# Kernel tuning notes

Hardware: AMD Instinct MI355X
Metric: run time of the kernel (lower is better)

The kernel has to match this reference:

```python
import jax, jax.numpy as jnp
import numpy as np
from math import factorial
from fractions import Fraction

MUL = 16          # multiplicity per irrep
LMAX = 2          # irreps l = 0, 1, 2
N_BATCH = 1024
RS = [(MUL, l, 0) for l in range(LMAX + 1)]   # Rs_1 = Rs_2


def _su2_cg_coeff(j1, m1, j2, m2, j3, m3):
    if m3 != m1 + m2:
        return 0.0
    f = factorial
    vmin = max(-j1 + j2 + m3, -j1 + m1, 0)
    vmax = min(j2 + j3 + m1, j3 - j1 + j2, j3 + m3)
    C = ((2 * j3 + 1) * Fraction(
        f(j3 + j1 - j2) * f(j3 - j1 + j2) * f(j1 + j2 - j3) * f(j3 + m3) * f(j3 - m3),
        f(j1 + j2 + j3 + 1) * f(j1 - m1) * f(j1 + m1) * f(j2 - m2) * f(j2 + m2))) ** 0.5
    S = 0
    for v in range(vmin, vmax + 1):
        S += (-1) ** (v + j2 + m2) * Fraction(
            f(j2 + j3 + m1 - v) * f(j1 - m1 + v),
            f(v) * f(j3 - j1 + j2 - v) * f(j3 + m3 - v) * f(v + j1 - j2 - m3))
    return float(C * S)


def _su2_cg(j1, j2, j3):
    mat = np.zeros((2 * j1 + 1, 2 * j2 + 1, 2 * j3 + 1))
    for m1 in range(-j1, j1 + 1):
        for m2 in range(-j2, j2 + 1):
            m3 = m1 + m2
            if abs(m3) <= j3:
                mat[j1 + m1, j2 + m2, j3 + m3] = _su2_cg_coeff(j1, m1, j2, m2, j3, m3)
    return mat


def _q_real_to_complex(l):
    q = np.zeros((2 * l + 1, 2 * l + 1), dtype=np.complex128)
    for m in range(-l, 0):
        q[l + m, l + abs(m)] = 2 ** -0.5
        q[l + m, l - abs(m)] = -1j * 2 ** -0.5
    q[l, l] = 1.0
    for m in range(1, l + 1):
        q[l + m, l + abs(m)] = (-1) ** m * 2 ** -0.5
        q[l + m, l - abs(m)] = 1j * (-1) ** m * 2 ** -0.5
    return (-1j) ** l * q


def _real_cg(l_out, l1, l2):
    # real-basis Wigner-3j block, shape (2*l_out+1, 2*l1+1, 2*l2+1)
    C = _su2_cg(l1, l2, l_out).astype(np.complex128)
    Q1, Q2, Q3 = _q_real_to_complex(l1), _q_real_to_complex(l2), _q_real_to_complex(l_out)
    C = np.einsum('ij,kl,mn,ikn->jlm', Q1, Q2, np.conj(Q3.T), C)
    C = np.real(C).transpose(2, 0, 1)   # -> (k, i, j)
    n = np.linalg.norm(C)
    assert n > 1e-8
    # wigner_3j has unit Frobenius norm; 'component' normalization multiplies by sqrt(2*l_out+1)
    return C / n * (2 * l_out + 1) ** 0.5


def _simplify(Rs):
    out = []
    for mul, l, p in Rs:
        if out and out[-1][1] == l and out[-1][2] == p:
            out[-1][0] += mul
        elif mul > 0:
            out.append([mul, l, p])
    return out


def _sort_dst(Rs):
    # stable sort of irrep blocks by (l, p); returns dst[old_row] = new_row
    xs, j = [], 0
    for mul, l, p in Rs:
        d = mul * (2 * l + 1)
        xs.append((l, p, mul, j, d))
        j += d
    dst = np.zeros(j, dtype=np.int64)
    i = 0
    for l, p, mul, jo, d in sorted(xs):
        dst[jo:jo + d] = np.arange(i, i + d)
        i += d
    return dst


def _build_sparse_tp(Rs1, Rs2):
    # replicates _tensor_product_in_in with the default selection rule
    rows, iis, jjs, vs = [], [], [], []
    Rs_out = []
    index_out = 0
    index_1 = 0
    for mul1, l1, p1 in Rs1:
        index_2 = 0
        for mul2, l2, p2 in Rs2:
            for l_out in range(abs(l1 - l2), l1 + l2 + 1):
                C = _real_cg(l_out, l1, l2)
                kc, ic, jc = np.nonzero(np.abs(C) > 1e-12)
                cv = C[kc, ic, jc]
                w = np.arange(mul1 * mul2)
                u, v = w // mul2, w % mul2
                rows.append((index_out + w[:, None] * (2 * l_out + 1) + kc[None, :]).ravel())
                iis.append((index_1 + u[:, None] * (2 * l1 + 1) + ic[None, :]).ravel())
                jjs.append((index_2 + v[:, None] * (2 * l2 + 1) + jc[None, :]).ravel())
                vs.append(np.tile(cv, mul1 * mul2))
                Rs_out.append([mul1 * mul2, l_out, p1 * p2])
                index_out += mul1 * mul2 * (2 * l_out + 1)
            index_2 += mul2 * (2 * l2 + 1)
        index_1 += mul1 * (2 * l1 + 1)
    k_idx = np.concatenate(rows)
    dst = _sort_dst(_simplify(Rs_out))   # sorted=True in the original module
    k_idx = dst[k_idx]
    return (k_idx, np.concatenate(iis), np.concatenate(jjs),
            np.concatenate(vs).astype(np.float32), index_out)


def setup_inputs() -> dict:
    key = jax.random.key(0)
    k1, k2 = jax.random.split(key)
    k_idx, i_idx, j_idx, vals, dim_out = _build_sparse_tp(RS, RS)
    dim_in = sum(mul * (2 * l + 1) for mul, l, _ in RS)   # 144
    x1 = jax.random.normal(k1, (N_BATCH, dim_in), dtype=jnp.float32)
    x2 = jax.random.normal(k2, (N_BATCH, dim_in), dtype=jnp.float32)
    return {"x1": x1, "x2": x2,
            "vals": jnp.asarray(vals),
            "k_idx": jnp.asarray(k_idx),
            "i_idx": jnp.asarray(i_idx),
            "j_idx": jnp.asarray(j_idx),
            "dim_out": int(dim_out)}


def reference(x1, x2, vals, k_idx, i_idx, j_idx, dim_out):
    # out[z, k] = sum_{nnz with row k} vals * x1[z, i] * x2[z, j]
    # (sparse Wigner-3j tensor contracted with the outer product of the inputs)
    prod = x1[:, i_idx] * x2[:, j_idx] * vals[None, :]               # [N, nnz]
    out = jax.ops.segment_sum(prod.T, k_idx, num_segments=dim_out)   # [dim_out, N]
    return out.T
```

## Files before the change

### kernel.cpp

```cpp
#include <hip/hip_runtime.h>


#define ZPT 16
#define BLK 256
#define DIM_IN 144

__global__ void seg_bounds_kernel(const int* __restrict__ k_idx, int nnz,
                                  int* __restrict__ seg_start,
                                  int* __restrict__ seg_end) {
    int n = blockIdx.x * blockDim.x + threadIdx.x;
    if (n >= nnz) return;
    int k = k_idx[n];
    if (n == 0 || k_idx[n - 1] != k) seg_start[k] = n;
    if (n == nnz - 1 || k_idx[n + 1] != k) seg_end[k] = n + 1;
}

__global__ __launch_bounds__(BLK) void tp_kernel(
        const float* __restrict__ x1,
        const float* __restrict__ x2,
        const float* __restrict__ vals,
        const int* __restrict__ i_idx,
        const int* __restrict__ j_idx,
        const int* __restrict__ seg_start,
        const int* __restrict__ seg_end,
        float* __restrict__ out,
        int dim_out, int n_batch) {
    __shared__ float x1s[ZPT * DIM_IN];
    __shared__ float x2s[ZPT * DIM_IN];

    const int z0 = blockIdx.y * ZPT;

    {
        const float4* s1 = (const float4*)(x1 + (size_t)z0 * DIM_IN);
        const float4* s2 = (const float4*)(x2 + (size_t)z0 * DIM_IN);
        float4* d1 = (float4*)x1s;
        float4* d2 = (float4*)x2s;
        const int n4 = ZPT * DIM_IN / 4;
        for (int t = threadIdx.x; t < n4; t += BLK) {
            d1[t] = s1[t];
            d2[t] = s2[t];
        }
    }
    __syncthreads();

    const int k = blockIdx.x * BLK + threadIdx.x;
    if (k >= dim_out) return;

    const int s = seg_start[k];
    const int e = seg_end[k];

    float acc[ZPT];
#pragma unroll
    for (int t = 0; t < ZPT; ++t) acc[t] = 0.0f;

    for (int n = s; n < e; ++n) {
        const float c = vals[n];
        const int i = i_idx[n];
        const int j = j_idx[n];
#pragma unroll
        for (int t = 0; t < ZPT; ++t) {
            acc[t] += c * x1s[t * DIM_IN + i] * x2s[t * DIM_IN + j];
        }
    }

#pragma unroll
    for (int t = 0; t < ZPT; ++t) {
        out[(size_t)(z0 + t) * dim_out + k] = acc[t];
    }
}

extern "C" void kernel_launch(void* const* d_in, const int* in_sizes, int n_in,
                              void* d_out, int out_size, void* d_ws, size_t ws_size,
                              hipStream_t stream) {
    const float* x1   = (const float*)d_in[0];
    const float* x2   = (const float*)d_in[1];
    const float* vals = (const float*)d_in[2];
    const int*   kidx = (const int*)d_in[3];
    const int*   iidx = (const int*)d_in[4];
    const int*   jidx = (const int*)d_in[5];
    float* out = (float*)d_out;

    const int n_batch = 1024;
    const int dim_out = out_size / n_batch;
    const int nnz     = in_sizes[2];

    int* seg_start = (int*)d_ws;
    int* seg_end   = seg_start + dim_out;

    hipMemsetAsync(d_ws, 0, (size_t)2 * dim_out * sizeof(int), stream);

    {
        int grid = (nnz + BLK - 1) / BLK;
        seg_bounds_kernel<<<grid, BLK, 0, stream>>>(kidx, nnz, seg_start, seg_end);
    }

    {
        dim3 grid((dim_out + BLK - 1) / BLK, n_batch / ZPT);
        tp_kernel<<<grid, BLK, 0, stream>>>(x1, x2, vals, iidx, jidx,
                                            seg_start, seg_end, out,
                                            dim_out, n_batch);
    }
}
```

Baseline: 33.22 us.

## Transpose shared inputs for float4 reads, pack sparse entries, drop memset

```diff
diff --git a/kernel.cpp b/kernel.cpp
--- a/kernel.cpp
+++ b/kernel.cpp
@@ -2,44 +2,53 @@
 
 
 #define ZPT 16
-#define BLK 256
+#define BLK 512
 #define DIM_IN 144
+#define STRIDE 20
 
-__global__ void seg_bounds_kernel(const int* __restrict__ k_idx, int nnz,
-                                  int* __restrict__ seg_start,
-                                  int* __restrict__ seg_end) {
+__global__ void prep_kernel(const int* __restrict__ k_idx,
+                            const float* __restrict__ vals,
+                            const int* __restrict__ i_idx,
+                            const int* __restrict__ j_idx,
+                            int nnz,
+                            int* __restrict__ seg_start,
+                            int* __restrict__ seg_end,
+                            int2* __restrict__ packed) {
     int n = blockIdx.x * blockDim.x + threadIdx.x;
     if (n >= nnz) return;
     int k = k_idx[n];
     if (n == 0 || k_idx[n - 1] != k) seg_start[k] = n;
     if (n == nnz - 1 || k_idx[n + 1] != k) seg_end[k] = n + 1;
+    packed[n] = make_int2(i_idx[n] | (j_idx[n] << 16), __float_as_int(vals[n]));
 }
 
 __global__ __launch_bounds__(BLK) void tp_kernel(
         const float* __restrict__ x1,
         const float* __restrict__ x2,
-        const float* __restrict__ vals,
-        const int* __restrict__ i_idx,
-        const int* __restrict__ j_idx,
+        const int2* __restrict__ packed,
         const int* __restrict__ seg_start,
         const int* __restrict__ seg_end,
         float* __restrict__ out,
-        int dim_out, int n_batch) {
-    __shared__ float x1s[ZPT * DIM_IN];
-    __shared__ float x2s[ZPT * DIM_IN];
+        int dim_out) {
+    __shared__ __align__(16) float x1s[DIM_IN * STRIDE];
+    __shared__ __align__(16) float x2s[DIM_IN * STRIDE];
 
     const int z0 = blockIdx.y * ZPT;
 
-    {
-        const float4* s1 = (const float4*)(x1 + (size_t)z0 * DIM_IN);
-        const float4* s2 = (const float4*)(x2 + (size_t)z0 * DIM_IN);
-        float4* d1 = (float4*)x1s;
-        float4* d2 = (float4*)x2s;
-        const int n4 = ZPT * DIM_IN / 4;
-        for (int t = threadIdx.x; t < n4; t += BLK) {
-            d1[t] = s1[t];
-            d2[t] = s2[t];
-        }
+    for (int idx = threadIdx.x; idx < ZPT * (DIM_IN / 4); idx += BLK) {
+        const int t  = idx / (DIM_IN / 4);
+        const int i4 = idx % (DIM_IN / 4);
+        const float4 a = *(const float4*)(x1 + (size_t)(z0 + t) * DIM_IN + i4 * 4);
+        const float4 b = *(const float4*)(x2 + (size_t)(z0 + t) * DIM_IN + i4 * 4);
+        const int base = i4 * 4 * STRIDE + t;
+        x1s[base             ] = a.x;
+        x1s[base +     STRIDE] = a.y;
+        x1s[base + 2 * STRIDE] = a.z;
+        x1s[base + 3 * STRIDE] = a.w;
+        x2s[base             ] = b.x;
+        x2s[base +     STRIDE] = b.y;
+        x2s[base + 2 * STRIDE] = b.z;
+        x2s[base + 3 * STRIDE] = b.w;
     }
     __syncthreads();
 
@@ -54,12 +63,20 @@
     for (int t = 0; t < ZPT; ++t) acc[t] = 0.0f;
 
     for (int n = s; n < e; ++n) {
-        const float c = vals[n];
-        const int i = i_idx[n];
-        const int j = j_idx[n];
+        const int2 ev = packed[n];
+        const float c = __int_as_float(ev.y);
+        const int i = ev.x & 0xffff;
+        const int j = ev.x >> 16;
+        const float4* p1 = (const float4*)(x1s + i * STRIDE);
+        const float4* p2 = (const float4*)(x2s + j * STRIDE);
 #pragma unroll
-        for (int t = 0; t < ZPT; ++t) {
-            acc[t] += c * x1s[t * DIM_IN + i] * x2s[t * DIM_IN + j];
+        for (int q = 0; q < 4; ++q) {
+            const float4 a = p1[q];
+            const float4 b = p2[q];
+            acc[4 * q + 0] += c * a.x * b.x;
+            acc[4 * q + 1] += c * a.y * b.y;
+            acc[4 * q + 2] += c * a.z * b.z;
+            acc[4 * q + 3] += c * a.w * b.w;
         }
     }
 
@@ -84,20 +101,19 @@
     const int dim_out = out_size / n_batch;
     const int nnz     = in_sizes[2];
 
-    int* seg_start = (int*)d_ws;
-    int* seg_end   = seg_start + dim_out;
-
-    hipMemsetAsync(d_ws, 0, (size_t)2 * dim_out * sizeof(int), stream);
+    int*  seg_start = (int*)d_ws;
+    int*  seg_end   = seg_start + dim_out;
+    int2* packed    = (int2*)(seg_end + dim_out);
 
     {
-        int grid = (nnz + BLK - 1) / BLK;
-        seg_bounds_kernel<<<grid, BLK, 0, stream>>>(kidx, nnz, seg_start, seg_end);
+        int grid = (nnz + 255) / 256;
+        prep_kernel<<<grid, 256, 0, stream>>>(kidx, vals, iidx, jidx, nnz,
+                                              seg_start, seg_end, packed);
     }
 
     {
         dim3 grid((dim_out + BLK - 1) / BLK, n_batch / ZPT);
-        tp_kernel<<<grid, BLK, 0, stream>>>(x1, x2, vals, iidx, jidx,
-                                            seg_start, seg_end, out,
-                                            dim_out, n_batch);
+        tp_kernel<<<grid, BLK, 0, stream>>>(x1, x2, packed,
+                                            seg_start, seg_end, out, dim_out);
     }
 }
```

Result: faster. 30.11 us (-9.4%).
